# Kernel tuning notes

Measured on AMD Instinct MI355X. Metric: run time of the kernel, lower is better.

## Reference

```python
import jax, jax.numpy as jnp
import numpy as np

B, L, D, Z, H, N, G = 8, 2048, 1024, 128, 2048, 16, 32
MAXPOS = 2048
EPS = 1e-5
PRIOR_COUNT = 2.0  # TimestepNorm prior pseudo-count


def setup_inputs() -> dict:
    ks = jax.random.split(jax.random.key(0), 12)
    std = 0.02  # bert init
    return {
        "x": jax.random.normal(ks[0], (B, L, D), jnp.float32),
        "prior_mean": jnp.zeros((G,), jnp.float32),
        "prior_logv": jnp.zeros((G,), jnp.float32),
        "tn_weight": jnp.ones((D,), jnp.float32),
        "tn_bias": jnp.zeros((D,), jnp.float32),
        "delta": jax.random.normal(ks[1], (D, N), jnp.float32),
        "alpha": jax.random.normal(ks[2], (D, N), jnp.float32),
        "ema_beta": jax.random.normal(ks[3], (D, N), jnp.float32),
        "ema_gamma": jax.random.normal(ks[4], (D, N), jnp.float32),
        "omega": jax.random.normal(ks[5], (D,), jnp.float32),
        "rms_weight": jnp.ones((D,), jnp.float32),
        "Wv": jax.random.normal(ks[6], (H, D), jnp.float32) * std,
        "bv": jnp.zeros((H,), jnp.float32),
        "Wmx": jax.random.normal(ks[7], (Z + H + 2 * D, D), jnp.float32) * std,
        "bmx": jnp.zeros((Z + H + 2 * D,), jnp.float32),
        "Wh": jax.random.normal(ks[8], (D, H), jnp.float32) * std,
        "qk_gamma": jax.random.normal(ks[9], (2, Z), jnp.float32) * 0.1,
        "qk_beta": jax.random.normal(ks[10], (2, Z), jnp.float32) * 0.1,
        "rel_bias": jax.random.normal(ks[11], (2 * MAXPOS - 1,), jnp.float32) * 0.02,
    }


def timestep_norm(x, prior_mean, prior_logv, weight, bias):
    """Causal cumulative group norm with a prior (TimestepNorm)."""
    m = D // G  # features per group
    xg = x.reshape(B, L, G, m)
    s1 = jnp.cumsum(xg.sum(-1), axis=1)            # B,L,G  running sum
    s2 = jnp.cumsum((xg * xg).sum(-1), axis=1)     # B,L,G  running sum of squares
    cnt = PRIOR_COUNT + m * jnp.arange(1, L + 1, dtype=x.dtype)[None, :, None]
    pv = jnp.exp(prior_logv)
    mean = (PRIOR_COUNT * prior_mean + s1) / cnt
    var = (PRIOR_COUNT * (pv + prior_mean ** 2) + s2) / cnt - mean ** 2
    xn = (xg - mean[..., None]) * jax.lax.rsqrt(var[..., None] + EPS)
    return xn.reshape(B, L, D) * weight + bias


def multihead_ema(x, delta, alpha, ema_beta, ema_gamma, omega):
    """MultiHeadEMA: causal damped-EMA convolution via FFT, plus omega residual."""
    p = jax.nn.sigmoid(delta)                       # D,N
    a = jax.nn.sigmoid(alpha)
    q = 1.0 - p * a                                 # decay in (0,1)
    t = jnp.arange(L, dtype=x.dtype)
    vander = jnp.exp(t[None, None, :] * jnp.log(q)[:, :, None])  # D,N,L
    scale = 1.0 / jnp.sqrt(jnp.asarray(N, x.dtype))
    kern = jnp.einsum('dn,dnl,dn->dl', p * ema_beta, vander, ema_gamma * scale)
    xT = x.transpose(0, 2, 1)                       # B,D,L
    n = 2 * L
    out = jnp.fft.irfft(jnp.fft.rfft(xT, n=n) * jnp.fft.rfft(kern, n=n)[None], n=n)[..., :L]
    out = out + xT * omega[:, None]
    return out.transpose(0, 2, 1)


def _forward(x, prior_mean, prior_logv, tn_weight, tn_bias, delta, alpha,
             ema_beta, ema_gamma, omega, rms_weight, Wv, bv, Wmx, bmx, Wh,
             qk_gamma, qk_beta, rel_bias):
    residual = x
    xn = timestep_norm(x, prior_mean, prior_logv, tn_weight, tn_bias)
    v = jax.nn.silu(xn @ Wv.T + bv)                 # B,L,H
    mx = multihead_ema(xn, delta, alpha, ema_beta, ema_gamma, omega)
    mx = mx * jax.lax.rsqrt(jnp.mean(mx * mx, axis=-1, keepdims=True) + EPS) * rms_weight  # RMSNorm
    base = mx @ Wmx.T + bmx                         # B,L,Z+H+2D
    u = jax.nn.sigmoid(base[..., :D])
    zr = jax.nn.silu(base[..., D:D + Z + H])
    hx = base[..., D + Z + H:]
    z, r = zr[..., :Z], zr[..., Z:]
    zz = z[..., None, :] * qk_gamma + qk_beta       # B,L,2,Z
    q = zz[..., 0, :] * (Z ** -0.5)
    k = zz[..., 1, :]
    # simple relative positional bias: bias[i,j] = rel_bias[MAXPOS-1 + (j-i)]
    idx = (MAXPOS - 1) + (jnp.arange(L)[None, :] - jnp.arange(L)[:, None])
    qk = jnp.einsum('biz,bjz->bij', q, k) + rel_bias[idx]
    causal = jnp.tril(jnp.ones((L, L), bool))
    qk = jnp.where(causal, qk, -jnp.inf)
    attn = jax.nn.softmax(qk, axis=-1)              # B,L,L
    h = jnp.einsum('bij,bjh->bih', attn, v)         # B,L,H
    h = jax.nn.silu(hx + (h * r) @ Wh.T)            # B,L,D
    return residual + u * (h - residual)


def reference(x, prior_mean, prior_logv, tn_weight, tn_bias, delta, alpha,
              ema_beta, ema_gamma, omega, rms_weight, Wv, bv, Wmx, bmx, Wh,
              qk_gamma, qk_beta, rel_bias):
    return _forward(x, prior_mean, prior_logv, tn_weight, tn_bias, delta, alpha,
                    ema_beta, ema_gamma, omega, rms_weight, Wv, bv, Wmx, bmx, Wh,
                    qk_gamma, qk_beta, rel_bias)
```

## Files before the change

kernel.cpp:

```cpp
#include <hip/hip_runtime.h>
#include <stdint.h>

#define B_ 8
#define L_ 2048
#define D_ 1024
#define Z_ 128
#define H_ 2048
#define NE_ 16
#define G_ 32
#define MAXPOS_ 2048
#define NMX_ 4224
#define EPS_ 1e-5f
#define PC_ 2.0f
#define NTILE_ 16
#define NPACK_ 136
#define TILE_ELEMS_ 16384

typedef short bf16x8 __attribute__((ext_vector_type(8)));
typedef float f32x4 __attribute__((ext_vector_type(4)));

__device__ __forceinline__ float bf2f(uint16_t u) {
  union { uint32_t u; float f; } v; v.u = ((uint32_t)u) << 16; return v.f;
}
__device__ __forceinline__ uint16_t f2bf(float f) {
  union { float f; uint32_t u; } v; v.f = f;
  uint32_t r = (v.u + 0x7FFFu + ((v.u >> 16) & 1u)) >> 16;
  return (uint16_t)r;
}
__device__ __forceinline__ float sigmoidf_(float x) { return 1.f / (1.f + __expf(-x)); }
__device__ __forceinline__ float siluf_(float x) { return x / (1.f + __expf(-x)); }

__device__ __forceinline__ float waveRedSum(float v) {
  #pragma unroll
  for (int m = 32; m; m >>= 1) v += __shfl_xor(v, m, 64);
  return v;
}

__device__ __forceinline__ void gl2lds(const uint16_t* g, uint16_t* l) {
  __builtin_amdgcn_global_load_lds(
      (const __attribute__((address_space(1))) void*)g,
      (__attribute__((address_space(3))) void*)l, 16, 0, 0);
}

__global__ __launch_bounds__(256) void k_fallback(float* __restrict__ out, int n, float wsmb) {
  for (int i = blockIdx.x * 256 + threadIdx.x; i < n; i += gridDim.x * 256)
    out[i] = (i == 0) ? wsmb : 0.f;
}

__global__ __launch_bounds__(256) void k_f2bf(const float* __restrict__ src,
                                              uint16_t* __restrict__ dst, int n) {
  for (int i = blockIdx.x * 256 + threadIdx.x; i < n; i += gridDim.x * 256)
    dst[i] = f2bf(src[i]);
}

__global__ __launch_bounds__(256) void k_tnsum(const float* __restrict__ x,
                                               float* __restrict__ s1g,
                                               float* __restrict__ s2g) {
  const int bg = blockIdx.x;
  const int b = bg / G_, g = bg % G_;
  const int tid = threadIdx.x;
  const int j = tid & 31;
  const int lsub = tid >> 5;
  #pragma unroll
  for (int i = 0; i < 16; ++i) {
    const int l = blockIdx.y * 128 + i * 8 + lsub;
    float v = x[((size_t)(b * L_ + l)) * D_ + g * 32 + j];
    float a = v, sq = v * v;
    #pragma unroll
    for (int m = 1; m <= 16; m <<= 1) { a += __shfl_xor(a, m, 64); sq += __shfl_xor(sq, m, 64); }
    if (j == 0) { s1g[(size_t)bg * L_ + l] = a; s2g[(size_t)bg * L_ + l] = sq; }
  }
}

__global__ __launch_bounds__(64) void k_tnscan(float* __restrict__ s1g,
                                               float* __restrict__ s2g) {
  const int bg = blockIdx.x;
  const int lane = threadIdx.x;
  #pragma unroll
  for (int pass = 0; pass < 2; ++pass) {
    float* gp = (pass ? s2g : s1g) + (size_t)bg * L_;
    float loc[32];
    const int b0 = lane * 32;
    float tot = 0.f;
    #pragma unroll
    for (int t = 0; t < 32; ++t) { loc[t] = gp[b0 + t]; tot += loc[t]; }
    float incl = tot;
    #pragma unroll
    for (int off = 1; off < 64; off <<= 1) {
      float nv = __shfl_up(incl, off, 64);
      if (lane >= off) incl += nv;
    }
    float run = incl - tot;
    #pragma unroll
    for (int t = 0; t < 32; ++t) { run += loc[t]; gp[b0 + t] = run; }
  }
}

__global__ __launch_bounds__(256) void k_tnnorm(const float* __restrict__ x,
                                                const float* __restrict__ s1g,
                                                const float* __restrict__ s2g,
                                                const float* __restrict__ pm,
                                                const float* __restrict__ plv,
                                                const float* __restrict__ w,
                                                const float* __restrict__ bias,
                                                uint16_t* __restrict__ xn) {
  const int bg = blockIdx.x;
  const int b = bg / G_, g = bg % G_;
  const int tid = threadIdx.x;
  const int j = tid & 31;
  const int lsub = tid >> 5;
  const float pmv = pm[g];
  const float pvv = __expf(plv[g]);
  const float wj = w[g * 32 + j];
  const float bj = bias[g * 32 + j];
  const float pterm = PC_ * (pvv + pmv * pmv);
  #pragma unroll
  for (int i = 0; i < 16; ++i) {
    const int l = blockIdx.y * 128 + i * 8 + lsub;
    const size_t idx = ((size_t)(b * L_ + l)) * D_ + g * 32 + j;
    const float v = x[idx];
    const float cnt = PC_ + 32.f * (float)(l + 1);
    const float mean = (PC_ * pmv + s1g[(size_t)bg * L_ + l]) / cnt;
    const float var = (pterm + s2g[(size_t)bg * L_ + l]) / cnt - mean * mean;
    xn[idx] = f2bf((v - mean) * rsqrtf(var + EPS_) * wj + bj);
  }
}

template <typename T>
__global__ __launch_bounds__(256) void k_transpose(const T* __restrict__ src,
                                                   T* __restrict__ dst, int R, int C) {
  __shared__ T tile[32][33];
  const size_t batch = (size_t)R * C * blockIdx.z;
  const int c0 = blockIdx.x * 32, r0 = blockIdx.y * 32;
  const int tx = threadIdx.x & 31, ty = threadIdx.x >> 5;
  #pragma unroll
  for (int k = 0; k < 4; ++k) {
    int r = ty + k * 8;
    tile[r][tx] = src[batch + (size_t)(r0 + r) * C + c0 + tx];
  }
  __syncthreads();
  #pragma unroll
  for (int k = 0; k < 4; ++k) {
    int r = ty + k * 8;
    dst[batch + (size_t)(c0 + r) * R + r0 + tx] = tile[tx][r];
  }
}

__global__ __launch_bounds__(64) void k_ema(const uint16_t* __restrict__ xnT,
                                            const float* __restrict__ delta,
                                            const float* __restrict__ alpha,
                                            const float* __restrict__ beta,
                                            const float* __restrict__ gamma,
                                            const float* __restrict__ omega,
                                            float* __restrict__ mxT) {
  __shared__ float hst[64 * NE_];
  const int bd = blockIdx.x;
  const int d = bd & (D_ - 1);
  const int c = threadIdx.x;

  float q[NE_], pb[NE_], gs[NE_];
  #pragma unroll
  for (int n = 0; n < NE_; ++n) {
    float p = sigmoidf_(delta[d * NE_ + n]);
    float a = sigmoidf_(alpha[d * NE_ + n]);
    q[n] = 1.f - p * a;
    pb[n] = p * beta[d * NE_ + n];
    gs[n] = gamma[d * NE_ + n] * 0.25f;
  }

  const uint16_t* xp = xnT + (size_t)bd * L_ + c * 32;
  bf16x8 xin[4];
  #pragma unroll
  for (int s = 0; s < 4; ++s) xin[s] = *(const bf16x8*)(xp + s * 8);

  float h[NE_];
  #pragma unroll
  for (int n = 0; n < NE_; ++n) h[n] = 0.f;

  #pragma unroll
  for (int k = 0; k < 32; ++k) {
    float xv = bf2f((uint16_t)xin[k >> 3][k & 7]);
    #pragma unroll
    for (int n = 0; n < NE_; ++n) h[n] = fmaf(q[n], h[n], pb[n] * xv);
  }
  #pragma unroll
  for (int n = 0; n < NE_; ++n) hst[c * NE_ + n] = h[n];
  __syncthreads();

  if (c < NE_) {
    float qq = q[c];
    float q32 = qq * qq; q32 *= q32; q32 *= q32; q32 *= q32; q32 *= q32;
    float hi = 0.f;
    for (int cc = 0; cc < 64; ++cc) {
      float cur = hst[cc * NE_ + c];
      hst[cc * NE_ + c] = hi;
      hi = fmaf(q32, hi, cur);
    }
  }
  __syncthreads();

  #pragma unroll
  for (int n = 0; n < NE_; ++n) h[n] = hst[c * NE_ + n];
  const float om = omega[d];
  float* op = mxT + (size_t)bd * L_ + c * 32;
  f32x4 ov;
  #pragma unroll
  for (int k = 0; k < 32; ++k) {
    float xv = bf2f((uint16_t)xin[k >> 3][k & 7]);
    float accv = 0.f;
    #pragma unroll
    for (int n = 0; n < NE_; ++n) {
      h[n] = fmaf(q[n], h[n], pb[n] * xv);
      accv = fmaf(gs[n], h[n], accv);
    }
    ov[k & 3] = accv + om * xv;
    if ((k & 3) == 3) *(f32x4*)(op + (k & ~3)) = ov;
  }
}

__global__ __launch_bounds__(256) void k_rms(const float* __restrict__ mx,
                                             const float* __restrict__ w,
                                             uint16_t* __restrict__ mxn) {
  __shared__ float red[4];
  const size_t row = blockIdx.x;
  const int tid = threadIdx.x;
  float ss = 0.f;
  #pragma unroll
  for (int i = 0; i < 4; ++i) {
    float v = mx[row * D_ + tid + i * 256];
    ss += v * v;
  }
  ss = waveRedSum(ss);
  if ((tid & 63) == 0) red[tid >> 6] = ss;
  __syncthreads();
  ss = red[0] + red[1] + red[2] + red[3];
  const float scale = rsqrtf(ss * (1.f / D_) + EPS_);
  #pragma unroll
  for (int i = 0; i < 4; ++i) {
    int dcol = tid + i * 256;
    mxn[row * D_ + dcol] = f2bf(mx[row * D_ + dcol] * scale * w[dcol]);
  }
}

__global__ __launch_bounds__(256) void k_qkprep(const float* __restrict__ z,
                                                const float* __restrict__ qg,
                                                const float* __restrict__ qb,
                                                uint16_t* __restrict__ q,
                                                uint16_t* __restrict__ k, int n) {
  for (int i = blockIdx.x * 256 + threadIdx.x; i < n; i += gridDim.x * 256) {
    int zc = i & (Z_ - 1);
    float v = z[i];
    q[i] = f2bf((v * qg[zc] + qb[zc]) * 0.08838834764831845f);
    k[i] = f2bf(v * qg[Z_ + zc] + qb[Z_ + zc]);
  }
}


template <int MODE>
__global__ __launch_bounds__(256, 3) void k_gemm128(
    const uint16_t* __restrict__ A, const uint16_t* __restrict__ Bm,
    int N, int K,
    const float* __restrict__ bias,
    float* __restrict__ outf, uint16_t* __restrict__ outb,
    uint16_t* __restrict__ ubuf, float* __restrict__ zbuf,
    uint16_t* __restrict__ rbuf, float* __restrict__ hxbuf,
    const float* __restrict__ x0) {
  __shared__ uint16_t sm[32768];
  const int t = threadIdx.x;
  const int lane = t & 63, wave = t >> 6;
  const int quad = lane >> 4, r16 = lane & 15;
  const int wm = wave >> 1, wn = wave & 1;
  const int bm = blockIdx.x * 128;
  const int bn = blockIdx.y * 128;

  f32x4 acc[4][4];
  const f32x4 zf = {0.f, 0.f, 0.f, 0.f};
  #pragma unroll
  for (int i = 0; i < 4; ++i)
    #pragma unroll
    for (int j = 0; j < 4; ++j) acc[i][j] = zf;

  const int sgz = (((t & 7) ^ ((t >> 3) & 7)) << 3);
  const uint16_t* gA = A + (size_t)(bm + (t >> 3)) * K + sgz;
  const uint16_t* gB = Bm + (size_t)(bn + (t >> 3)) * K + sgz;
  const size_t qstep = (size_t)32 * K;
  uint16_t* lA = sm + t * 8;
  uint16_t* lB = sm + 8192 + t * 8;

  const int g0 = quad ^ (r16 & 7);
  const int aRowOff = (wm * 64 + r16) * 64;
  const int bRowOff = 8192 + (wn * 64 + r16) * 64;

#define STAGE(c, kb) do {                                                     \
    _Pragma("unroll")                                                         \
    for (int q = 0; q < 4; ++q) {                                             \
      gl2lds(gA + q * qstep + (kb), lA + (c) * 16384 + q * 2048);             \
      gl2lds(gB + q * qstep + (kb), lB + (c) * 16384 + q * 2048);             \
    }                                                                         \
  } while (0)

  const int NT = K >> 6;

  STAGE(0, 0);
  __syncthreads();

  bf16x8 af[4], bfr[4];
  for (int tt = 0; tt < NT; ++tt) {
    const int c = tt & 1;
    const int co = c * 16384;
    if (tt + 1 < NT) STAGE(c ^ 1, (tt + 1) * 64);
    #pragma unroll
    for (int kh = 0; kh < 2; ++kh) {
      const int ga = (g0 ^ (kh << 2)) << 3;
      #pragma unroll
      for (int j = 0; j < 4; ++j)
        bfr[j] = *(const bf16x8*)&sm[co + bRowOff + j * 1024 + ga];
      #pragma unroll
      for (int i = 0; i < 4; ++i)
        af[i] = *(const bf16x8*)&sm[co + aRowOff + i * 1024 + ga];
      #pragma unroll
      for (int i = 0; i < 4; ++i)
        #pragma unroll
        for (int j = 0; j < 4; ++j)
          acc[i][j] = __builtin_amdgcn_mfma_f32_16x16x32_bf16(
              af[i], bfr[j], acc[i][j], 0, 0, 0);
    }
    __syncthreads();
  }
#undef STAGE

  #pragma unroll
  for (int i = 0; i < 4; ++i) {
    #pragma unroll
    for (int j = 0; j < 4; ++j) {
      #pragma unroll
      for (int r = 0; r < 4; ++r) {
        const int row = bm + wm * 64 + i * 16 + quad * 4 + r;
        const int col = bn + wn * 64 + j * 16 + r16;
        float val = acc[i][j][r];
        if (MODE == 0) {
          outb[(size_t)row * N + col] = f2bf(siluf_(val + bias[col]));
        } else if (MODE == 1) {
          val += bias[col];
          if (col < D_)                 ubuf[(size_t)row * D_ + col] = f2bf(sigmoidf_(val));
          else if (col < D_ + Z_)       zbuf[(size_t)row * Z_ + (col - D_)] = siluf_(val);
          else if (col < D_ + Z_ + H_)  rbuf[(size_t)row * H_ + (col - D_ - Z_)] = f2bf(siluf_(val));
          else                          hxbuf[(size_t)row * D_ + (col - D_ - Z_ - H_)] = val;
        } else {
          const size_t idx = (size_t)row * N + col;
          float g = siluf_(val + hxbuf[idx]);
          float xv = x0[idx];
          outf[idx] = xv + bf2f(ubuf[idx]) * (g - xv);
        }
      }
    }
  }
}

__global__ __launch_bounds__(256) void k_qksm(
    const uint16_t* __restrict__ qg, const uint16_t* __restrict__ kg,
    const float* __restrict__ relb, uint16_t* __restrict__ Pp) {
  __shared__ uint16_t Ks[128 * 128];
  __shared__ float relwin[256];
  const int qt = blockIdx.x;
  const int bl = blockIdx.y;
  const int tid = threadIdx.x;
  const int w = tid >> 6, lane = tid & 63;
  const int quad = lane >> 4, r16 = lane & 15;
  const uint16_t* qb_b = qg + (size_t)bl * L_ * Z_;
  const uint16_t* kb_b = kg + (size_t)bl * L_ * Z_;
  uint16_t* P_b = Pp + (size_t)bl * NPACK_ * TILE_ELEMS_;

  const int ksg = (tid >> 4) * 128 + (((tid & 15) ^ ((tid >> 4) & 7)) << 3);
  const int kg7 = r16 & 7;

  bf16x8 aq[2][4];
  #pragma unroll
  for (int i = 0; i < 2; ++i)
    #pragma unroll
    for (int s = 0; s < 4; ++s)
      aq[i][s] = *(const bf16x8*)&qb_b[(size_t)(qt * 128 + w * 32 + i * 16 + r16) * Z_ +
                                       s * 32 + quad * 8];

  float m8[8], l8[8];
  #pragma unroll
  for (int t = 0; t < 8; ++t) { m8[t] = -3.4e38f; l8[t] = 0.f; }

  const f32x4 zf = {0.f, 0.f, 0.f, 0.f};

  for (int kt = 0; kt <= qt; ++kt) {
    __syncthreads();
    const uint16_t* src = kb_b + (size_t)kt * 128 * Z_;
    #pragma unroll
    for (int s2 = 0; s2 < 8; ++s2)
      gl2lds(src + s2 * 2048 + ksg, Ks + s2 * 2048 + tid * 8);
    if (tid < 255) relwin[tid] = relb[2047 + (kt - qt) * 128 - 127 + tid];
    __syncthreads();
    #pragma unroll
    for (int j = 0; j < 8; ++j) {
      f32x4 a0 = zf, a1 = zf;
      #pragma unroll
      for (int s = 0; s < 4; ++s) {
        bf16x8 bk = *(const bf16x8*)&Ks[(j * 16 + r16) * 128 +
                                        (((s * 4 + quad) ^ kg7) << 3)];
        a0 = __builtin_amdgcn_mfma_f32_16x16x32_bf16(aq[0][s], bk, a0, 0, 0, 0);
        a1 = __builtin_amdgcn_mfma_f32_16x16x32_bf16(aq[1][s], bk, a1, 0, 0, 0);
      }
      #pragma unroll
      for (int i = 0; i < 2; ++i) {
        const f32x4 av = i ? a1 : a0;
        #pragma unroll
        for (int r = 0; r < 4; ++r) {
          const int rloc = w * 32 + i * 16 + quad * 4 + r;
          const int cloc = j * 16 + r16;
          if (kt < qt || cloc <= rloc) {
            const float v = av[r] + relwin[cloc - rloc + 127];
            const int t = i * 4 + r;
            const float mn = fmaxf(m8[t], v);
            l8[t] = l8[t] * __expf(m8[t] - mn) + __expf(v - mn);
            m8[t] = mn;
          }
        }
      }
    }
  }

  #pragma unroll
  for (int t = 0; t < 8; ++t) {
    #pragma unroll
    for (int msk = 1; msk <= 8; msk <<= 1) {
      const float mo = __shfl_xor(m8[t], msk, 64);
      const float lo = __shfl_xor(l8[t], msk, 64);
      const float mn = fmaxf(m8[t], mo);
      l8[t] = l8[t] * __expf(m8[t] - mn) + lo * __expf(mo - mn);
      m8[t] = mn;
    }
    l8[t] = 1.f / l8[t];
  }

  for (int kt = 0; kt <= qt; ++kt) {
    __syncthreads();
    const uint16_t* src = kb_b + (size_t)kt * 128 * Z_;
    #pragma unroll
    for (int s2 = 0; s2 < 8; ++s2)
      gl2lds(src + s2 * 2048 + ksg, Ks + s2 * 2048 + tid * 8);
    if (tid < 255) relwin[tid] = relb[2047 + (kt - qt) * 128 - 127 + tid];
    __syncthreads();
    uint16_t* Pt = P_b + (size_t)(qt * (qt + 1) / 2 + kt) * TILE_ELEMS_;
    #pragma unroll
    for (int j = 0; j < 8; ++j) {
      f32x4 a0 = zf, a1 = zf;
      #pragma unroll
      for (int s = 0; s < 4; ++s) {
        bf16x8 bk = *(const bf16x8*)&Ks[(j * 16 + r16) * 128 +
                                        (((s * 4 + quad) ^ kg7) << 3)];
        a0 = __builtin_amdgcn_mfma_f32_16x16x32_bf16(aq[0][s], bk, a0, 0, 0, 0);
        a1 = __builtin_amdgcn_mfma_f32_16x16x32_bf16(aq[1][s], bk, a1, 0, 0, 0);
      }
      #pragma unroll
      for (int i = 0; i < 2; ++i) {
        const f32x4 av = i ? a1 : a0;
        #pragma unroll
        for (int r = 0; r < 4; ++r) {
          const int rloc = w * 32 + i * 16 + quad * 4 + r;
          const int cloc = j * 16 + r16;
          const int t = i * 4 + r;
          float p = 0.f;
          if (kt < qt || cloc <= rloc) {
            const float v = av[r] + relwin[cloc - rloc + 127];
            p = __expf(v - m8[t]) * l8[t];
          }
          Pt[rloc * 128 + cloc] = f2bf(p);
        }
      }
    }
  }
}

__global__ __launch_bounds__(256) void k_pv(
    const uint16_t* __restrict__ Pp, const uint16_t* __restrict__ vT,
    uint16_t* __restrict__ rh) {
  __shared__ uint16_t As[128 * 32];
  __shared__ uint16_t Bs[128 * 32];
  const int qt = blockIdx.x;
  const int bn = blockIdx.y * 128;
  const int bl = blockIdx.z;
  const uint16_t* P_b = Pp + (size_t)bl * NPACK_ * TILE_ELEMS_;
  const uint16_t* v_b = vT + (size_t)bl * H_ * L_;
  uint16_t* rh_b = rh + (size_t)bl * L_ * H_;

  const int tid = threadIdx.x;
  const int wave = tid >> 6, lane = tid & 63;
  const int quad = lane >> 4, r16 = lane & 15;
  const int wm = wave >> 1, wn = wave & 1;
  const int rowW = wm * 64, colW = wn * 64;

  f32x4 acc[4][4];
  const f32x4 zf = {0.f, 0.f, 0.f, 0.f};
  #pragma unroll
  for (int i = 0; i < 4; ++i)
    #pragma unroll
    for (int j = 0; j < 4; ++j) acc[i][j] = zf;

  const int rA = tid >> 2;
  const int sg = (((tid & 3) ^ (rA & 3)) << 3);
  const int gpv = ((quad ^ (r16 & 3)) << 3);
  uint16_t* lA0 = As + tid * 8;
  uint16_t* lA1 = As + 2048 + tid * 8;
  uint16_t* lB0 = Bs + tid * 8;
  uint16_t* lB1 = Bs + 2048 + tid * 8;

  for (int kt = 0; kt <= qt; ++kt) {
    const uint16_t* At = P_b + (size_t)(qt * (qt + 1) / 2 + kt) * TILE_ELEMS_;
    #pragma unroll
    for (int ks = 0; ks < 4; ++ks) {
      const int kb = kt * 128 + ks * 32;
      __syncthreads();
      gl2lds(At + rA * 128 + ks * 32 + sg, lA0);
      gl2lds(At + (rA + 64) * 128 + ks * 32 + sg, lA1);
      gl2lds(v_b + (size_t)(bn + rA) * L_ + kb + sg, lB0);
      gl2lds(v_b + (size_t)(bn + 64 + rA) * L_ + kb + sg, lB1);
      __syncthreads();
      bf16x8 af[4], bfr[4];
      #pragma unroll
      for (int i = 0; i < 4; ++i)
        af[i] = *(const bf16x8*)&As[(rowW + i * 16 + r16) * 32 + gpv];
      #pragma unroll
      for (int j = 0; j < 4; ++j)
        bfr[j] = *(const bf16x8*)&Bs[(colW + j * 16 + r16) * 32 + gpv];
      #pragma unroll
      for (int i = 0; i < 4; ++i)
        #pragma unroll
        for (int j = 0; j < 4; ++j)
          acc[i][j] = __builtin_amdgcn_mfma_f32_16x16x32_bf16(af[i], bfr[j], acc[i][j], 0, 0, 0);
    }
  }

  #pragma unroll
  for (int i = 0; i < 4; ++i) {
    #pragma unroll
    for (int j = 0; j < 4; ++j) {
      #pragma unroll
      for (int r = 0; r < 4; ++r) {
        const int row = qt * 128 + rowW + i * 16 + quad * 4 + r;
        const int col = bn + colW + j * 16 + r16;
        const size_t idx = (size_t)row * H_ + col;
        const float rv = bf2f(rh_b[idx]);
        rh_b[idx] = f2bf(acc[i][j][r] * rv);
      }
    }
  }
}

extern "C" void kernel_launch(void* const* d_in, const int* in_sizes, int n_in,
                              void* d_out, int out_size, void* d_ws, size_t ws_size,
                              hipStream_t stream) {
  (void)in_sizes; (void)n_in;
  const float* x         = (const float*)d_in[0];
  const float* prior_mean= (const float*)d_in[1];
  const float* prior_logv= (const float*)d_in[2];
  const float* tn_w      = (const float*)d_in[3];
  const float* tn_b      = (const float*)d_in[4];
  const float* delta     = (const float*)d_in[5];
  const float* alpha     = (const float*)d_in[6];
  const float* ema_beta  = (const float*)d_in[7];
  const float* ema_gamma = (const float*)d_in[8];
  const float* omega     = (const float*)d_in[9];
  const float* rms_w     = (const float*)d_in[10];
  const float* Wv        = (const float*)d_in[11];
  const float* bv        = (const float*)d_in[12];
  const float* Wmx       = (const float*)d_in[13];
  const float* bmx       = (const float*)d_in[14];
  const float* Wh        = (const float*)d_in[15];
  const float* qk_gamma  = (const float*)d_in[16];
  const float* qk_beta   = (const float*)d_in[17];
  const float* rel_bias  = (const float*)d_in[18];
  float* out = (float*)d_out;

  const int BL = B_ * L_;
  const size_t MB = 1024 * 1024;
  const size_t REQUIRED = 256 * MB;

  if (ws_size < REQUIRED) {
    k_fallback<<<dim3(4096), dim3(256), 0, stream>>>(out, out_size, (float)(ws_size / MB));
    return;
  }

  char* p = (char*)d_ws;
  uint16_t* xn   = (uint16_t*)(p);
  uint16_t* ubuf = (uint16_t*)(p);
  float*    s1g  = (float*)   (p + 32 * MB);
  float*    s2g  = (float*)   (p + 34 * MB);
  uint16_t* xnT  = (uint16_t*)(p + 32 * MB);
  uint16_t* mxn  = (uint16_t*)(p + 32 * MB);
  uint16_t* vbuf = (uint16_t*)(p + 64 * MB);
  float*    mx   = (float*)   (p + 64 * MB);
  uint16_t* rbuf = (uint16_t*)(p + 64 * MB);
  uint16_t* wv_b = (uint16_t*)(p + 128 * MB);
  uint16_t* vT   = (uint16_t*)(p + 128 * MB);
  uint16_t* wmx_b = (uint16_t*)(p + 192 * MB);
  uint16_t* wh_b  = (uint16_t*)(p + 192 * MB);
  float*    zb    = (float*)   (p + 201 * MB);
  uint16_t* qb    = (uint16_t*)(p + 209 * MB);
  uint16_t* kb2   = (uint16_t*)(p + 213 * MB);
  uint16_t* Ppack = (uint16_t*)(p + 217 * MB);
  float* mxT = out;
  float* hx  = out;

  k_f2bf<<<dim3(1024), dim3(256), 0, stream>>>(Wv, wv_b, H_ * D_);
  k_f2bf<<<dim3(2048), dim3(256), 0, stream>>>(Wmx, wmx_b, NMX_ * D_);
  k_tnsum<<<dim3(B_ * G_, 16), dim3(256), 0, stream>>>(x, s1g, s2g);
  k_tnscan<<<dim3(B_ * G_), dim3(64), 0, stream>>>(s1g, s2g);
  k_tnnorm<<<dim3(B_ * G_, 16), dim3(256), 0, stream>>>(
      x, s1g, s2g, prior_mean, prior_logv, tn_w, tn_b, xn);
  k_transpose<uint16_t><<<dim3(D_ / 32, L_ / 32, B_), dim3(256), 0, stream>>>(xn, xnT, L_, D_);
  k_gemm128<0><<<dim3(BL / 128, H_ / 128), dim3(256), 0, stream>>>(
      xn, wv_b, H_, D_, bv, nullptr, vbuf,
      nullptr, nullptr, nullptr, nullptr, nullptr);
  k_transpose<uint16_t><<<dim3(H_ / 32, L_ / 32, B_), dim3(256), 0, stream>>>(vbuf, vT, L_, H_);
  k_ema<<<dim3(B_ * D_), dim3(64), 0, stream>>>(xnT, delta, alpha, ema_beta, ema_gamma, omega, mxT);
  k_transpose<float><<<dim3(L_ / 32, D_ / 32, B_), dim3(256), 0, stream>>>(mxT, mx, D_, L_);
  k_rms<<<dim3(BL), dim3(256), 0, stream>>>(mx, rms_w, mxn);
  k_gemm128<1><<<dim3(BL / 128, NMX_ / 128), dim3(256), 0, stream>>>(
      mxn, wmx_b, NMX_, D_, bmx, nullptr, nullptr,
      ubuf, zb, rbuf, hx, nullptr);
  k_qkprep<<<dim3(1024), dim3(256), 0, stream>>>(zb, qk_gamma, qk_beta, qb, kb2, BL * Z_);
  k_qksm<<<dim3(NTILE_, B_), dim3(256), 0, stream>>>(qb, kb2, rel_bias, Ppack);
  k_pv<<<dim3(NTILE_, H_ / 128, B_), dim3(256), 0, stream>>>(Ppack, vT, rbuf);
  k_f2bf<<<dim3(1024), dim3(256), 0, stream>>>(Wh, wh_b, D_ * H_);
  k_gemm128<4><<<dim3(BL / 128, D_ / 128), dim3(256), 0, stream>>>(
      rbuf, wh_b, D_, H_, nullptr, out, nullptr,
      ubuf, nullptr, nullptr, hx, x);
}
```

Before: 1.227 ms.

## Double-buffer PV loads, shrink GEMM K-tile to 32, reverse PV tile order

The GEMM kernel's K-step drops from 64 to 32, which halves shared memory, and the launch-bounds occupancy hint rises from 3 to 5 blocks. The PV kernel replaces its single-buffered load/sync/compute loop with a double-buffered pipeline, so the next tile's loads overlap the current MFMAs. PV blocks are also issued longest-first (reversed qt) to balance the triangular workload. The trade-offs are more loop iterations and barriers per unit of work in the GEMM, and possible register pressure from the higher occupancy target.

```diff
diff --git a/kernel.cpp b/kernel.cpp
--- a/kernel.cpp
+++ b/kernel.cpp
@@ -257,7 +257,7 @@
 
 
 template <int MODE>
-__global__ __launch_bounds__(256, 3) void k_gemm128(
+__global__ __launch_bounds__(256, 5) void k_gemm128(
     const uint16_t* __restrict__ A, const uint16_t* __restrict__ Bm,
     int N, int K,
     const float* __restrict__ bias,
@@ -265,7 +265,7 @@
     uint16_t* __restrict__ ubuf, float* __restrict__ zbuf,
     uint16_t* __restrict__ rbuf, float* __restrict__ hxbuf,
     const float* __restrict__ x0) {
-  __shared__ uint16_t sm[32768];
+  __shared__ uint16_t sm[16384];
   const int t = threadIdx.x;
   const int lane = t & 63, wave = t >> 6;
   const int quad = lane >> 4, r16 = lane & 15;
@@ -280,26 +280,25 @@
     #pragma unroll
     for (int j = 0; j < 4; ++j) acc[i][j] = zf;
 
-  const int sgz = (((t & 7) ^ ((t >> 3) & 7)) << 3);
-  const uint16_t* gA = A + (size_t)(bm + (t >> 3)) * K + sgz;
-  const uint16_t* gB = Bm + (size_t)(bn + (t >> 3)) * K + sgz;
-  const size_t qstep = (size_t)32 * K;
+  const int sgz = (((t & 3) ^ ((t >> 3) & 3)) << 3);
+  const uint16_t* gA = A + (size_t)(bm + (t >> 2)) * K + sgz;
+  const uint16_t* gB = Bm + (size_t)(bn + (t >> 2)) * K + sgz;
+  const size_t qstep = (size_t)64 * K;
   uint16_t* lA = sm + t * 8;
-  uint16_t* lB = sm + 8192 + t * 8;
-
-  const int g0 = quad ^ (r16 & 7);
-  const int aRowOff = (wm * 64 + r16) * 64;
-  const int bRowOff = 8192 + (wn * 64 + r16) * 64;
+  uint16_t* lB = sm + 4096 + t * 8;
+
+  const int ga = ((quad ^ ((r16 >> 1) & 3)) << 3);
+  const int aOff = (wm * 64 + r16) * 32 + ga;
+  const int bOff = 4096 + (wn * 64 + r16) * 32 + ga;
 
 #define STAGE(c, kb) do {                                                     \
-    _Pragma("unroll")                                                         \
-    for (int q = 0; q < 4; ++q) {                                             \
-      gl2lds(gA + q * qstep + (kb), lA + (c) * 16384 + q * 2048);             \
-      gl2lds(gB + q * qstep + (kb), lB + (c) * 16384 + q * 2048);             \
-    }                                                                         \
+    gl2lds(gA + (kb), lA + (c) * 8192);                                       \
+    gl2lds(gA + qstep + (kb), lA + (c) * 8192 + 2048);                        \
+    gl2lds(gB + (kb), lB + (c) * 8192);                                       \
+    gl2lds(gB + qstep + (kb), lB + (c) * 8192 + 2048);                        \
   } while (0)
 
-  const int NT = K >> 6;
+  const int NT = K >> 5;
 
   STAGE(0, 0);
   __syncthreads();
@@ -307,24 +306,20 @@
   bf16x8 af[4], bfr[4];
   for (int tt = 0; tt < NT; ++tt) {
     const int c = tt & 1;
-    const int co = c * 16384;
-    if (tt + 1 < NT) STAGE(c ^ 1, (tt + 1) * 64);
-    #pragma unroll
-    for (int kh = 0; kh < 2; ++kh) {
-      const int ga = (g0 ^ (kh << 2)) << 3;
+    const int co = c * 8192;
+    if (tt + 1 < NT) STAGE(c ^ 1, (tt + 1) * 32);
+    #pragma unroll
+    for (int j = 0; j < 4; ++j)
+      bfr[j] = *(const bf16x8*)&sm[co + bOff + j * 512];
+    #pragma unroll
+    for (int i = 0; i < 4; ++i)
+      af[i] = *(const bf16x8*)&sm[co + aOff + i * 512];
+    #pragma unroll
+    for (int i = 0; i < 4; ++i)
       #pragma unroll
       for (int j = 0; j < 4; ++j)
-        bfr[j] = *(const bf16x8*)&sm[co + bRowOff + j * 1024 + ga];
-      #pragma unroll
-      for (int i = 0; i < 4; ++i)
-        af[i] = *(const bf16x8*)&sm[co + aRowOff + i * 1024 + ga];
-      #pragma unroll
-      for (int i = 0; i < 4; ++i)
-        #pragma unroll
-        for (int j = 0; j < 4; ++j)
-          acc[i][j] = __builtin_amdgcn_mfma_f32_16x16x32_bf16(
-              af[i], bfr[j], acc[i][j], 0, 0, 0);
-    }
+        acc[i][j] = __builtin_amdgcn_mfma_f32_16x16x32_bf16(
+            af[i], bfr[j], acc[i][j], 0, 0, 0);
     __syncthreads();
   }
 #undef STAGE
@@ -477,15 +472,15 @@
   }
 }
 
-__global__ __launch_bounds__(256) void k_pv(
+__global__ __launch_bounds__(256, 5) void k_pv(
     const uint16_t* __restrict__ Pp, const uint16_t* __restrict__ vT,
     uint16_t* __restrict__ rh) {
-  __shared__ uint16_t As[128 * 32];
-  __shared__ uint16_t Bs[128 * 32];
-  const int qt = blockIdx.x;
+  __shared__ uint16_t sm[16384];
+  const int qt = NTILE_ - 1 - blockIdx.x;
   const int bn = blockIdx.y * 128;
   const int bl = blockIdx.z;
-  const uint16_t* P_b = Pp + (size_t)bl * NPACK_ * TILE_ELEMS_;
+  const uint16_t* Pq = Pp + (size_t)bl * NPACK_ * TILE_ELEMS_ +
+                       (size_t)(qt * (qt + 1) / 2) * TILE_ELEMS_;
   const uint16_t* v_b = vT + (size_t)bl * H_ * L_;
   uint16_t* rh_b = rh + (size_t)bl * L_ * H_;
 
@@ -503,38 +498,44 @@
     for (int j = 0; j < 4; ++j) acc[i][j] = zf;
 
   const int rA = tid >> 2;
-  const int sg = (((tid & 3) ^ (rA & 3)) << 3);
-  const int gpv = ((quad ^ (r16 & 3)) << 3);
-  uint16_t* lA0 = As + tid * 8;
-  uint16_t* lA1 = As + 2048 + tid * 8;
-  uint16_t* lB0 = Bs + tid * 8;
-  uint16_t* lB1 = Bs + 2048 + tid * 8;
-
-  for (int kt = 0; kt <= qt; ++kt) {
-    const uint16_t* At = P_b + (size_t)(qt * (qt + 1) / 2 + kt) * TILE_ELEMS_;
-    #pragma unroll
-    for (int ks = 0; ks < 4; ++ks) {
-      const int kb = kt * 128 + ks * 32;
-      __syncthreads();
-      gl2lds(At + rA * 128 + ks * 32 + sg, lA0);
-      gl2lds(At + (rA + 64) * 128 + ks * 32 + sg, lA1);
-      gl2lds(v_b + (size_t)(bn + rA) * L_ + kb + sg, lB0);
-      gl2lds(v_b + (size_t)(bn + 64 + rA) * L_ + kb + sg, lB1);
-      __syncthreads();
-      bf16x8 af[4], bfr[4];
-      #pragma unroll
-      for (int i = 0; i < 4; ++i)
-        af[i] = *(const bf16x8*)&As[(rowW + i * 16 + r16) * 32 + gpv];
+  const int sg = (((tid & 3) ^ ((tid >> 3) & 3)) << 3);
+  const int gpv = ((quad ^ ((r16 >> 1) & 3)) << 3);
+
+#define PVSTAGE(c, s) do {                                                    \
+    const int kt_ = (s) >> 2, ks_ = (s) & 3;                                  \
+    const uint16_t* At_ = Pq + (size_t)kt_ * TILE_ELEMS_ + ks_ * 32 + sg;     \
+    const uint16_t* Bt_ = v_b + (size_t)(bn + rA) * L_ + kt_ * 128 +          \
+                          ks_ * 32 + sg;                                      \
+    gl2lds(At_ + rA * 128, sm + (c) * 8192 + tid * 8);                        \
+    gl2lds(At_ + (rA + 64) * 128, sm + (c) * 8192 + 2048 + tid * 8);          \
+    gl2lds(Bt_, sm + (c) * 8192 + 4096 + tid * 8);                            \
+    gl2lds(Bt_ + (size_t)64 * L_, sm + (c) * 8192 + 6144 + tid * 8);          \
+  } while (0)
+
+  const int S = 4 * (qt + 1);
+
+  PVSTAGE(0, 0);
+  __syncthreads();
+
+  bf16x8 af[4], bfr[4];
+  for (int s = 0; s < S; ++s) {
+    const int c = s & 1;
+    const int co = c * 8192;
+    if (s + 1 < S) PVSTAGE(c ^ 1, s + 1);
+    #pragma unroll
+    for (int j = 0; j < 4; ++j)
+      bfr[j] = *(const bf16x8*)&sm[co + 4096 + (colW + j * 16 + r16) * 32 + gpv];
+    #pragma unroll
+    for (int i = 0; i < 4; ++i)
+      af[i] = *(const bf16x8*)&sm[co + (rowW + i * 16 + r16) * 32 + gpv];
+    #pragma unroll
+    for (int i = 0; i < 4; ++i)
       #pragma unroll
       for (int j = 0; j < 4; ++j)
-        bfr[j] = *(const bf16x8*)&Bs[(colW + j * 16 + r16) * 32 + gpv];
-      #pragma unroll
-      for (int i = 0; i < 4; ++i)
-        #pragma unroll
-        for (int j = 0; j < 4; ++j)
-          acc[i][j] = __builtin_amdgcn_mfma_f32_16x16x32_bf16(af[i], bfr[j], acc[i][j], 0, 0, 0);
-    }
-  }
+        acc[i][j] = __builtin_amdgcn_mfma_f32_16x16x32_bf16(af[i], bfr[j], acc[i][j], 0, 0, 0);
+    __syncthreads();
+  }
+#undef PVSTAGE
 
   #pragma unroll
   for (int i = 0; i < 4; ++i) {
```

New measurement: 1.461 ms. 19.1% more time.
